# Kernel optimization log

Measured on AMD Instinct MI355X. Metric: run time of the kernel, lower is better.

The kernel has to match this reference:

```python
import jax, jax.numpy as jnp
import numpy as np

TEMP = 0.1
EPS = 1e-9  # torch CosineSimilarity eps


def setup_inputs() -> dict:
    key = jax.random.key(0)
    k1, k2 = jax.random.split(key)
    h = jax.random.normal(k1, (16384, 2048), dtype=jnp.float32)
    W = jax.random.normal(k2, (512, 2048), dtype=jnp.float32) * (1.0 / np.sqrt(2048))
    return {"h": h, "W": W}


def reference(h, W):
    # process_reps: h already 2D -> identity. Split into anchor / context halves.
    B = h.shape[0] // 2
    wz = h[:B] @ W.T      # [B, low_rank_dim]
    wc = h[B:] @ W.T      # [B, low_rank_dim]

    # CosineSimilarity(dim=-1, eps=1e-9): dot / max(||z||*||c||, eps), pairwise BxB
    nz = jnp.linalg.norm(wz, axis=-1)  # [B]
    nc = jnp.linalg.norm(wc, axis=-1)  # [B]
    sim = (wz @ wc.T) / jnp.maximum(nz[:, None] * nc[None, :], EPS)  # [B, B]
    sim = sim / TEMP

    sim_mean = sim.mean()
    sim_pos = jnp.diagonal(sim).mean()
    logprob = -jax.nn.log_softmax(sim, axis=1)
    loss = jnp.diagonal(logprob).mean()
    # matches loss_dict entries: {'loss', 'loss_pos', 'loss_neg'}
    return jnp.stack([loss, sim_pos, sim_mean])
```

## Files before the change

kernel.cpp:

```cpp
#include <hip/hip_runtime.h>


typedef __attribute__((ext_vector_type(8))) short bf16x8;
typedef __attribute__((ext_vector_type(4))) float floatx4;
typedef unsigned char uchar;

__device__ __forceinline__ unsigned short f2bf(float f) {
    union { float f; unsigned u; } v; v.f = f;
    unsigned r = (v.u + 0x7FFFu + ((v.u >> 16) & 1u)) >> 16;
    return (unsigned short)r;
}

__device__ __forceinline__ void async_copy16(const void* g, void* l) {
    __builtin_amdgcn_global_load_lds(
        (const __attribute__((address_space(1))) void*)g,
        (__attribute__((address_space(3))) void*)l,
        16, 0, 0);
}

__device__ __forceinline__ void cvt16(const float4* f, uchar* dst) {
    int4 pk;
    pk.x = (__builtin_amdgcn_cvt_pk_fp8_f32(f[0].x, f[0].y, 0, 0) & 0xffff)
         | (__builtin_amdgcn_cvt_pk_fp8_f32(f[0].z, f[0].w, 0, 0) << 16);
    pk.y = (__builtin_amdgcn_cvt_pk_fp8_f32(f[1].x, f[1].y, 0, 0) & 0xffff)
         | (__builtin_amdgcn_cvt_pk_fp8_f32(f[1].z, f[1].w, 0, 0) << 16);
    pk.z = (__builtin_amdgcn_cvt_pk_fp8_f32(f[2].x, f[2].y, 0, 0) & 0xffff)
         | (__builtin_amdgcn_cvt_pk_fp8_f32(f[2].z, f[2].w, 0, 0) << 16);
    pk.w = (__builtin_amdgcn_cvt_pk_fp8_f32(f[3].x, f[3].y, 0, 0) & 0xffff)
         | (__builtin_amdgcn_cvt_pk_fp8_f32(f[3].z, f[3].w, 0, 0) << 16);
    *reinterpret_cast<int4*>(dst) = pk;
}

__global__ __launch_bounds__(256) void cast_fp8_kernel(
    const float* __restrict__ src, uchar* __restrict__ dst, int n, float scale)
{
    const int i = (blockIdx.x * 256 + threadIdx.x) * 8;
    if (i + 7 < n) {
        float4 a = *reinterpret_cast<const float4*>(src + i);
        float4 b = *reinterpret_cast<const float4*>(src + i + 4);
        const int p01 = __builtin_amdgcn_cvt_pk_fp8_f32(a.x * scale, a.y * scale, 0, 0);
        const int p23 = __builtin_amdgcn_cvt_pk_fp8_f32(a.z * scale, a.w * scale, 0, 0);
        const int p45 = __builtin_amdgcn_cvt_pk_fp8_f32(b.x * scale, b.y * scale, 0, 0);
        const int p67 = __builtin_amdgcn_cvt_pk_fp8_f32(b.z * scale, b.w * scale, 0, 0);
        int2 w;
        w.x = (p01 & 0xffff) | (p23 << 16);
        w.y = (p45 & 0xffff) | (p67 << 16);
        *reinterpret_cast<int2*>(dst + i) = w;
    }
}

__device__ __forceinline__ size_t fl_off(int row_g, int col_g) {
    const int g = row_g >> 4, r15 = row_g & 15;
    const int c = col_g >> 5, q = (col_g >> 3) & 3, b = col_g & 7;
    return ((size_t)g * 16 + c) * 512 + (size_t)(q * 16 + r15) * 8 + b;
}

#define G1F_BODY(K, FC, FN, AR, BR, AW, BW, VM, STAGE_B, STAGE_H)              \
  {                                                                            \
    asm volatile("s_waitcnt vmcnt(" #VM ")" ::: "memory");                     \
    asm volatile("s_waitcnt lgkmcnt(0)" ::: "memory");                         \
    __builtin_amdgcn_s_barrier();                                              \
    __builtin_amdgcn_sched_barrier(0);                                         \
    long av[2][4], bv[2][8];                                                   \
    _Pragma("unroll")                                                          \
    for (int c = 0; c < 2; c++) {                                              \
      _Pragma("unroll")                                                        \
      for (int i = 0; i < 4; i++)                                              \
        av[c][i] = *reinterpret_cast<const long*>(AR + fA + i * 1024 + c * 32);\
      _Pragma("unroll")                                                        \
      for (int j = 0; j < 8; j++)                                              \
        bv[c][j] = *reinterpret_cast<const long*>(BR + fB + j * 1024 + c * 32);\
    }                                                                          \
    __builtin_amdgcn_s_setprio(1);                                             \
    _Pragma("unroll")                                                          \
    for (int c = 0; c < 2; c++)                                                \
      _Pragma("unroll")                                                        \
      for (int i = 0; i < 4; i++)                                              \
        _Pragma("unroll")                                                      \
        for (int j = 0; j < 8; j++)                                            \
          acc[i][j] = __builtin_amdgcn_mfma_f32_16x16x32_fp8_fp8(              \
              av[c][i], bv[c][j], acc[i][j], 0, 0, 0);                         \
    __builtin_amdgcn_s_setprio(0);                                             \
    if (STAGE_B) {                                                             \
      _Pragma("unroll")                                                        \
      for (int s = 0; s < 8; s++)                                              \
        async_copy16(gBs + ((K) + 1) * 64 + s * 131072, BW + swave + s * 4096);\
      cvt16(FC, AW + aoff);                                                    \
    }                                                                          \
    if (STAGE_H) {                                                             \
      _Pragma("unroll")                                                        \
      for (int c4 = 0; c4 < 4; c4++)                                           \
        FN[c4] = *reinterpret_cast<const float4*>(gH + ((K) + 2) * 64 + c4 * 4);\
    }                                                                          \
  }

__global__ __launch_bounds__(256, 1) void g1f(
    const float* __restrict__ h, const uchar* __restrict__ W8,
    uchar* __restrict__ Z8F, float* __restrict__ norm2)
{
    __shared__ __align__(16) uchar As0[64 * 64],  As1[64 * 64];
    __shared__ __align__(16) uchar Bs0[512 * 64], Bs1[512 * 64];

    const int blk = blockIdx.x;
    const int t = threadIdx.x;
    const int wave = t >> 6, lane = t & 63;
    const int quad = lane >> 4, l15 = lane & 15;

    floatx4 acc[4][8];
    #pragma unroll
    for (int i = 0; i < 4; i++)
        #pragma unroll
        for (int j = 0; j < 8; j++) acc[i][j] = {0.f, 0.f, 0.f, 0.f};

    const int arow = t >> 2, ap = t & 3;
    const float* gH = h + (size_t)(blk * 64 + arow) * 2048 + ap * 16;
    const int aoff = arow * 64 + ap * 16;

    const uchar* gBs = W8 + (size_t)(wave * 16 + (lane >> 2)) * 2048 + (lane & 3) * 16;
    const int swave = wave * 1024;

    const int fA = l15 * 64 + quad * 8;
    const int fB = wave * 8192 + l15 * 64 + quad * 8;

    #pragma unroll
    for (int s = 0; s < 8; s++)
        async_copy16(gBs + s * 131072, Bs0 + swave + s * 4096);
    float4 p0[4], f0[4], f1[4];
    #pragma unroll
    for (int c = 0; c < 4; c++) p0[c] = *reinterpret_cast<const float4*>(gH + c * 4);
    #pragma unroll
    for (int c = 0; c < 4; c++) f1[c] = *reinterpret_cast<const float4*>(gH + 64 + c * 4);
    cvt16(p0, As0 + aoff);

    for (int kb = 0; kb < 15; kb++) {
        const int k = kb * 2;
        G1F_BODY(k,     f1, f0, As0, Bs0, As1, Bs1, 4, 1, 1)
        G1F_BODY(k + 1, f0, f1, As1, Bs1, As0, Bs0, 4, 1, 1)
    }
    G1F_BODY(30, f1, f0, As0, Bs0, As1, Bs1, 4, 1, 0)
    G1F_BODY(31, f0, f1, As1, Bs1, As0, Bs0, 0, 0, 0)

    #pragma unroll
    for (int i = 0; i < 4; i++) {
        #pragma unroll
        for (int r = 0; r < 4; r++) {
            const int row_g = blk * 64 + i * 16 + quad * 4 + r;
            float pw = 0.f;
            #pragma unroll
            for (int jp = 0; jp < 4; jp++) {
                const int pk = __builtin_amdgcn_cvt_pk_fp8_f32(
                    acc[i][2 * jp][r], acc[i][2 * jp + 1][r], 0, 0);
                Z8F[fl_off(row_g, wave * 128 + (2 * jp) * 16 + l15)]     = (uchar)(pk & 0xff);
                Z8F[fl_off(row_g, wave * 128 + (2 * jp + 1) * 16 + l15)] = (uchar)((pk >> 8) & 0xff);
                const float q0 = __builtin_amdgcn_cvt_f32_fp8(pk, 0);
                const float q1 = __builtin_amdgcn_cvt_f32_fp8(pk, 1);
                pw += q0 * q0 + q1 * q1;
            }
            pw += __shfl_xor(pw, 1, 16);
            pw += __shfl_xor(pw, 2, 16);
            pw += __shfl_xor(pw, 4, 16);
            pw += __shfl_xor(pw, 8, 16);
            if (l15 == 0) atomicAdd(&norm2[row_g], pw);
        }
    }
}

__global__ __launch_bounds__(256) void g1_slow(
    const float* __restrict__ h, const float* __restrict__ W,
    uchar* __restrict__ Z8F, float* __restrict__ norm2)
{
    __shared__ __align__(16) unsigned short As[128][40];
    __shared__ __align__(16) unsigned short Bs[128][40];

    const int bn = blockIdx.x, bm = blockIdx.y;
    const int t = threadIdx.x;
    const int wave = t >> 6, lane = t & 63;
    const int wm = wave & 1, wn = wave >> 1;
    const int quad = lane >> 4, l15 = lane & 15;

    floatx4 acc[4][4];
    #pragma unroll
    for (int i = 0; i < 4; i++)
        #pragma unroll
        for (int j = 0; j < 4; j++) acc[i][j] = {0.f, 0.f, 0.f, 0.f};

    const int lrow = t >> 1, lhalf = t & 1;
    const float* ga = h + (size_t)(bm * 128 + lrow) * 2048 + lhalf * 16;
    const float* gb = W + (size_t)(bn * 128 + lrow) * 2048 + lhalf * 16;

    for (int k0 = 0; k0 < 2048; k0 += 32) {
        #pragma unroll
        for (int c = 0; c < 4; c++) {
            const float4 va = *reinterpret_cast<const float4*>(ga + k0 + c * 4);
            const float4 vb = *reinterpret_cast<const float4*>(gb + k0 + c * 4);
            ushort4 ua = make_ushort4(f2bf(va.x), f2bf(va.y), f2bf(va.z), f2bf(va.w));
            ushort4 ub = make_ushort4(f2bf(vb.x), f2bf(vb.y), f2bf(vb.z), f2bf(vb.w));
            *reinterpret_cast<ushort4*>(&As[lrow][lhalf * 16 + c * 4]) = ua;
            *reinterpret_cast<ushort4*>(&Bs[lrow][lhalf * 16 + c * 4]) = ub;
        }
        __syncthreads();
        bf16x8 af[4], bfr[4];
        #pragma unroll
        for (int i = 0; i < 4; i++)
            af[i] = *reinterpret_cast<const bf16x8*>(&As[wm * 64 + i * 16 + l15][quad * 8]);
        #pragma unroll
        for (int j = 0; j < 4; j++)
            bfr[j] = *reinterpret_cast<const bf16x8*>(&Bs[wn * 64 + j * 16 + l15][quad * 8]);
        #pragma unroll
        for (int i = 0; i < 4; i++)
            #pragma unroll
            for (int j = 0; j < 4; j++)
                acc[i][j] = __builtin_amdgcn_mfma_f32_16x16x32_bf16(af[i], bfr[j], acc[i][j], 0, 0, 0);
        __syncthreads();
    }

    #pragma unroll
    for (int i = 0; i < 4; i++) {
        #pragma unroll
        for (int r = 0; r < 4; r++) {
            const int row_g = bm * 128 + wm * 64 + i * 16 + quad * 4 + r;
            const int pk01 = __builtin_amdgcn_cvt_pk_fp8_f32(acc[i][0][r], acc[i][1][r], 0, 0);
            const int pk23 = __builtin_amdgcn_cvt_pk_fp8_f32(acc[i][2][r], acc[i][3][r], 0, 0);
            const uchar q8[4] = { (uchar)(pk01 & 0xff), (uchar)((pk01 >> 8) & 0xff),
                                  (uchar)(pk23 & 0xff), (uchar)((pk23 >> 8) & 0xff) };
            #pragma unroll
            for (int j = 0; j < 4; j++) {
                const int col_g = bn * 128 + wn * 64 + j * 16 + l15;
                Z8F[fl_off(row_g, col_g)] = q8[j];
            }
            const float q0 = __builtin_amdgcn_cvt_f32_fp8(pk01, 0);
            const float q1 = __builtin_amdgcn_cvt_f32_fp8(pk01, 1);
            const float q2 = __builtin_amdgcn_cvt_f32_fp8(pk23, 0);
            const float q3 = __builtin_amdgcn_cvt_f32_fp8(pk23, 1);
            float pw = q0 * q0 + q1 * q1 + q2 * q2 + q3 * q3;
            pw += __shfl_xor(pw, 1, 16);
            pw += __shfl_xor(pw, 2, 16);
            pw += __shfl_xor(pw, 4, 16);
            pw += __shfl_xor(pw, 8, 16);
            if (l15 == 0) atomicAdd(&norm2[row_g], pw);
        }
    }
}

__global__ __launch_bounds__(256, 4) void g2_main(
    const uchar* __restrict__ Z8F, const float* __restrict__ norm2,
    float* __restrict__ rowse, float* __restrict__ bsum, float* __restrict__ bdiag)
{
    __shared__ __align__(16) uchar Bs[32768];
    __shared__ float red[8];
    float (*lds_red)[20] = (float (*)[20])(void*)Bs;

    const int o = blockIdx.y * 64 + blockIdx.x;
    const int xcd = o & 7, idx = o >> 3;
    const int bg = idx >> 7, r = idx & 127;
    const int bm = xcd * 8 + (r >> 4);
    const int bn = bg * 16 + (r & 15);
    const int t = threadIdx.x;
    const int wave = t >> 6, lane = t & 63;
    const int quad = lane >> 4, l15 = lane & 15;

    const uchar* gB = Z8F + (size_t)(512 + bn * 8) * 8192 + t * 16;
    #pragma unroll
    for (int s = 0; s < 8; s++)
        async_copy16(gB + s * 8192, &Bs[s * 4096 + wave * 1024]);

    floatx4 acc[2][8];
    #pragma unroll
    for (int i = 0; i < 2; i++)
        #pragma unroll
        for (int j = 0; j < 8; j++) acc[i][j] = {0.f, 0.f, 0.f, 0.f};

    const uchar* baseA = Z8F + (size_t)(bm * 8 + wave * 2) * 8192 + lane * 8;

    long ab[3][2];
    #pragma unroll
    for (int d = 0; d < 2; d++)
        #pragma unroll
        for (int i = 0; i < 2; i++)
            ab[d][i] = *reinterpret_cast<const long*>(baseA + i * 8192 + d * 512);

    __syncthreads();

    #pragma unroll
    for (int c = 0; c < 16; c++) {
        const int cl = c & 7;
        if (c < 14) {
            #pragma unroll
            for (int i = 0; i < 2; i++)
                ab[(c + 2) % 3][i] = *reinterpret_cast<const long*>(
                    baseA + i * 8192 + (c + 2) * 512);
        }
        long bb[8];
        #pragma unroll
        for (int j = 0; j < 8; j++)
            bb[j] = *reinterpret_cast<const long*>(&Bs[j * 4096 + cl * 512 + lane * 8]);
        __builtin_amdgcn_s_setprio(1);
        #pragma unroll
        for (int i = 0; i < 2; i++)
            #pragma unroll
            for (int j = 0; j < 8; j++)
                acc[i][j] = __builtin_amdgcn_mfma_f32_16x16x32_fp8_fp8(
                    ab[c % 3][i], bb[j], acc[i][j], 0, 0, 0);
        __builtin_amdgcn_s_setprio(0);
        if (c == 7) {
            __syncthreads();
            #pragma unroll
            for (int s = 0; s < 8; s++)
                async_copy16(gB + s * 8192 + 4096, &Bs[s * 4096 + wave * 1024]);
            __syncthreads();
        }
    }

    __syncthreads();

    float rc8[8];
    #pragma unroll
    for (int j = 0; j < 8; j++)
        rc8[j] = rsqrtf(fmaxf(norm2[8192 + bn * 128 + j * 16 + l15], 1e-30f));

    const bool diagblk = (bm == bn);
    float s_tot2 = 0.f, s_diag2 = 0.f;
    #pragma unroll
    for (int i = 0; i < 2; i++) {
        #pragma unroll
        for (int rr = 0; rr < 4; rr++) {
            const int row_t = wave * 32 + i * 16 + quad * 4 + rr;
            const float rzl2 = rsqrtf(fmaxf(norm2[bm * 128 + row_t], 1e-30f)) * 14.4269504089f;
            float rx = 0.f;
            #pragma unroll
            for (int j = 0; j < 8; j++) {
                const float sim2 = acc[i][j][rr] * rzl2 * rc8[j];
                s_tot2 += sim2;
                rx += exp2f(sim2);
                if (diagblk && j == wave * 2 + i && l15 == quad * 4 + rr)
                    s_diag2 += sim2;
            }
            lds_red[row_t][l15] = rx;
        }
    }
    __syncthreads();

    {
        const int row = t >> 1, half = t & 1;
        float v = 0.f;
        #pragma unroll
        for (int cc = 0; cc < 8; cc++) v += lds_red[row][half * 8 + cc];
        v += __shfl_xor(v, 1, 64);
        if (half == 0) atomicAdd(&rowse[bm * 128 + row], v);
    }

    #pragma unroll
    for (int off = 32; off; off >>= 1) {
        s_tot2  += __shfl_xor(s_tot2, off, 64);
        s_diag2 += __shfl_xor(s_diag2, off, 64);
    }
    if (lane == 0) { red[wave] = s_tot2; red[4 + wave] = s_diag2; }
    __syncthreads();
    if (t == 0) {
        bsum[bm * 64 + bn]  = (red[0] + red[1] + red[2] + red[3]) * 0.69314718056f;
        bdiag[bm * 64 + bn] = (red[4] + red[5] + red[6] + red[7]) * 0.69314718056f;
    }
}

__global__ __launch_bounds__(256) void finalize_kernel(
    const float* __restrict__ rowse, const float* __restrict__ bsum,
    const float* __restrict__ bdiag, float* __restrict__ out)
{
    float a = 0.f, b = 0.f, c = 0.f;
    for (int i = threadIdx.x; i < 8192; i += 256) a += logf(rowse[i]);
    for (int i = threadIdx.x; i < 4096; i += 256) { b += bsum[i]; c += bdiag[i]; }
    #pragma unroll
    for (int off = 32; off; off >>= 1) {
        a += __shfl_xor(a, off, 64);
        b += __shfl_xor(b, off, 64);
        c += __shfl_xor(c, off, 64);
    }
    __shared__ float ra[4], rb[4], rc[4];
    const int wave = threadIdx.x >> 6, lane = threadIdx.x & 63;
    if (lane == 0) { ra[wave] = a; rb[wave] = b; rc[wave] = c; }
    __syncthreads();
    if (threadIdx.x == 0) {
        const float A = ra[0] + ra[1] + ra[2] + ra[3];
        const float B = rb[0] + rb[1] + rb[2] + rb[3];
        const float C = rc[0] + rc[1] + rc[2] + rc[3];
        const float diag_mean = C / 8192.f;
        out[0] = A / 8192.f - diag_mean;
        out[1] = diag_mean;
        out[2] = B / (8192.f * 8192.f);
    }
}

extern "C" void kernel_launch(void* const* d_in, const int* in_sizes, int n_in,
                              void* d_out, int out_size, void* d_ws, size_t ws_size,
                              hipStream_t stream) {
    const float* h = (const float*)d_in[0];
    const float* W = (const float*)d_in[1];
    float* out = (float*)d_out;

    char* ws = (char*)d_ws;
    float* norm2 = (float*)(ws);
    float* rowse = (float*)(ws + 65536);
    float* bsum  = (float*)(ws + 98304);
    float* bdiag = (float*)(ws + 114688);
    uchar* Z8F   = (uchar*)(ws + 131072);
    uchar* W8    = (uchar*)(ws + 8519680);
    const size_t NEED_FAST = 9568256ull;

    hipMemsetAsync(ws, 0, 131072, stream);

    if (ws_size >= NEED_FAST) {
        const int nw = 512 * 2048;
        hipLaunchKernelGGL(cast_fp8_kernel, dim3(nw / 2048), dim3(256), 0, stream, W, W8, nw, 32.0f);
        hipLaunchKernelGGL(g1f, dim3(256), dim3(256), 0, stream, h, W8, Z8F, norm2);
    } else {
        hipLaunchKernelGGL(g1_slow, dim3(4, 128), dim3(256), 0, stream, h, W, Z8F, norm2);
    }
    hipLaunchKernelGGL(g2_main, dim3(64, 64), dim3(256), 0, stream, Z8F, norm2, rowse, bsum, bdiag);
    hipLaunchKernelGGL(finalize_kernel, dim3(1), dim3(256), 0, stream, rowse, bsum, bdiag, out);
}
```

Baseline: 317.8 us.

## Pre-swizzle W into MFMA fragment layout and read B directly from global

```diff
diff --git a/kernel.cpp b/kernel.cpp
--- a/kernel.cpp
+++ b/kernel.cpp
@@ -18,35 +18,13 @@
         16, 0, 0);
 }
 
-__device__ __forceinline__ void cvt16(const float4* f, uchar* dst) {
-    int4 pk;
+__device__ __forceinline__ void cvt8(const float4* f, uchar* dst) {
+    int2 pk;
     pk.x = (__builtin_amdgcn_cvt_pk_fp8_f32(f[0].x, f[0].y, 0, 0) & 0xffff)
          | (__builtin_amdgcn_cvt_pk_fp8_f32(f[0].z, f[0].w, 0, 0) << 16);
     pk.y = (__builtin_amdgcn_cvt_pk_fp8_f32(f[1].x, f[1].y, 0, 0) & 0xffff)
          | (__builtin_amdgcn_cvt_pk_fp8_f32(f[1].z, f[1].w, 0, 0) << 16);
-    pk.z = (__builtin_amdgcn_cvt_pk_fp8_f32(f[2].x, f[2].y, 0, 0) & 0xffff)
-         | (__builtin_amdgcn_cvt_pk_fp8_f32(f[2].z, f[2].w, 0, 0) << 16);
-    pk.w = (__builtin_amdgcn_cvt_pk_fp8_f32(f[3].x, f[3].y, 0, 0) & 0xffff)
-         | (__builtin_amdgcn_cvt_pk_fp8_f32(f[3].z, f[3].w, 0, 0) << 16);
-    *reinterpret_cast<int4*>(dst) = pk;
-}
-
-__global__ __launch_bounds__(256) void cast_fp8_kernel(
-    const float* __restrict__ src, uchar* __restrict__ dst, int n, float scale)
-{
-    const int i = (blockIdx.x * 256 + threadIdx.x) * 8;
-    if (i + 7 < n) {
-        float4 a = *reinterpret_cast<const float4*>(src + i);
-        float4 b = *reinterpret_cast<const float4*>(src + i + 4);
-        const int p01 = __builtin_amdgcn_cvt_pk_fp8_f32(a.x * scale, a.y * scale, 0, 0);
-        const int p23 = __builtin_amdgcn_cvt_pk_fp8_f32(a.z * scale, a.w * scale, 0, 0);
-        const int p45 = __builtin_amdgcn_cvt_pk_fp8_f32(b.x * scale, b.y * scale, 0, 0);
-        const int p67 = __builtin_amdgcn_cvt_pk_fp8_f32(b.z * scale, b.w * scale, 0, 0);
-        int2 w;
-        w.x = (p01 & 0xffff) | (p23 << 16);
-        w.y = (p45 & 0xffff) | (p67 << 16);
-        *reinterpret_cast<int2*>(dst + i) = w;
-    }
+    *reinterpret_cast<int2*>(dst) = pk;
 }
 
 __device__ __forceinline__ size_t fl_off(int row_g, int col_g) {
@@ -55,21 +33,46 @@
     return ((size_t)g * 16 + c) * 512 + (size_t)(q * 16 + r15) * 8 + b;
 }
 
-#define G1F_BODY(K, FC, FN, AR, BR, AW, BW, VM, STAGE_B, STAGE_H)              \
+__global__ __launch_bounds__(256) void cast_w_frag(
+    const float* __restrict__ W, uchar* __restrict__ W8F)
+{
+    const int i = (blockIdx.x * 256 + threadIdx.x) * 8;
+    const int r = i >> 11, k = i & 2047;
+    const float* s = W + (size_t)r * 2048 + k;
+    float4 a = *reinterpret_cast<const float4*>(s);
+    float4 b = *reinterpret_cast<const float4*>(s + 4);
+    int2 w;
+    w.x = (__builtin_amdgcn_cvt_pk_fp8_f32(a.x * 32.f, a.y * 32.f, 0, 0) & 0xffff)
+        | (__builtin_amdgcn_cvt_pk_fp8_f32(a.z * 32.f, a.w * 32.f, 0, 0) << 16);
+    w.y = (__builtin_amdgcn_cvt_pk_fp8_f32(b.x * 32.f, b.y * 32.f, 0, 0) & 0xffff)
+        | (__builtin_amdgcn_cvt_pk_fp8_f32(b.z * 32.f, b.w * 32.f, 0, 0) << 16);
+    const size_t off = (size_t)(r >> 4) * 32768 + (size_t)(k >> 5) * 512
+                     + (size_t)((k >> 3) & 3) * 128 + (size_t)(r & 15) * 8;
+    *reinterpret_cast<int2*>(W8F + off) = w;
+}
+
+#define G1R_ITER(K, AsR, AsW, FC, FN, DO_CVT, DO_LOAD)                         \
   {                                                                            \
-    asm volatile("s_waitcnt vmcnt(" #VM ")" ::: "memory");                     \
-    asm volatile("s_waitcnt lgkmcnt(0)" ::: "memory");                         \
-    __builtin_amdgcn_s_barrier();                                              \
-    __builtin_amdgcn_sched_barrier(0);                                         \
-    long av[2][4], bv[2][8];                                                   \
+    __syncthreads();                                                           \
+    long av[4][2];                                                             \
     _Pragma("unroll")                                                          \
-    for (int c = 0; c < 2; c++) {                                              \
+    for (int i = 0; i < 4; i++)                                                \
       _Pragma("unroll")                                                        \
-      for (int i = 0; i < 4; i++)                                              \
-        av[c][i] = *reinterpret_cast<const long*>(AR + fA + i * 1024 + c * 32);\
+      for (int c = 0; c < 2; c++)                                              \
+        av[i][c] = *reinterpret_cast<const long*>(                             \
+            AsR + (i * 16 + l15) * 64 +                                        \
+            (((c * 2 + (quad >> 1)) ^ (l15 & 3)) << 4) + (quad & 1) * 8);      \
+    long bb[4][2];                                                             \
+    _Pragma("unroll")                                                          \
+    for (int j = 0; j < 4; j++)                                                \
       _Pragma("unroll")                                                        \
-      for (int j = 0; j < 8; j++)                                              \
-        bv[c][j] = *reinterpret_cast<const long*>(BR + fB + j * 1024 + c * 32);\
+      for (int c = 0; c < 2; c++)                                              \
+        bb[j][c] = *reinterpret_cast<const long*>(                             \
+            gWF + j * 32768 + ((K) * 2 + c) * 512);                            \
+    if (DO_CVT) cvt8(FC, AsW + adst);                                          \
+    if (DO_LOAD) {                                                             \
+      FN[0] = *reinterpret_cast<const float4*>(gH + ((K) + 2) * 64);           \
+      FN[1] = *reinterpret_cast<const float4*>(gH + ((K) + 2) * 64 + 4);       \
     }                                                                          \
     __builtin_amdgcn_s_setprio(1);                                             \
     _Pragma("unroll")                                                          \
@@ -77,68 +80,49 @@
       _Pragma("unroll")                                                        \
       for (int i = 0; i < 4; i++)                                              \
         _Pragma("unroll")                                                      \
-        for (int j = 0; j < 8; j++)                                            \
+        for (int j = 0; j < 4; j++)                                            \
           acc[i][j] = __builtin_amdgcn_mfma_f32_16x16x32_fp8_fp8(              \
-              av[c][i], bv[c][j], acc[i][j], 0, 0, 0);                         \
+              av[i][c], bb[j][c], acc[i][j], 0, 0, 0);                         \
     __builtin_amdgcn_s_setprio(0);                                             \
-    if (STAGE_B) {                                                             \
-      _Pragma("unroll")                                                        \
-      for (int s = 0; s < 8; s++)                                              \
-        async_copy16(gBs + ((K) + 1) * 64 + s * 131072, BW + swave + s * 4096);\
-      cvt16(FC, AW + aoff);                                                    \
-    }                                                                          \
-    if (STAGE_H) {                                                             \
-      _Pragma("unroll")                                                        \
-      for (int c4 = 0; c4 < 4; c4++)                                           \
-        FN[c4] = *reinterpret_cast<const float4*>(gH + ((K) + 2) * 64 + c4 * 4);\
-    }                                                                          \
   }
 
-__global__ __launch_bounds__(256, 1) void g1f(
-    const float* __restrict__ h, const uchar* __restrict__ W8,
+__global__ __launch_bounds__(512, 2) void g1r(
+    const float* __restrict__ h, const uchar* __restrict__ W8F,
     uchar* __restrict__ Z8F, float* __restrict__ norm2)
 {
-    __shared__ __align__(16) uchar As0[64 * 64],  As1[64 * 64];
-    __shared__ __align__(16) uchar Bs0[512 * 64], Bs1[512 * 64];
+    __shared__ __align__(16) uchar As0[64 * 64], As1[64 * 64];
 
     const int blk = blockIdx.x;
     const int t = threadIdx.x;
     const int wave = t >> 6, lane = t & 63;
     const int quad = lane >> 4, l15 = lane & 15;
 
-    floatx4 acc[4][8];
+    floatx4 acc[4][4];
     #pragma unroll
     for (int i = 0; i < 4; i++)
         #pragma unroll
-        for (int j = 0; j < 8; j++) acc[i][j] = {0.f, 0.f, 0.f, 0.f};
-
-    const int arow = t >> 2, ap = t & 3;
-    const float* gH = h + (size_t)(blk * 64 + arow) * 2048 + ap * 16;
-    const int aoff = arow * 64 + ap * 16;
-
-    const uchar* gBs = W8 + (size_t)(wave * 16 + (lane >> 2)) * 2048 + (lane & 3) * 16;
-    const int swave = wave * 1024;
-
-    const int fA = l15 * 64 + quad * 8;
-    const int fB = wave * 8192 + l15 * 64 + quad * 8;
-
-    #pragma unroll
-    for (int s = 0; s < 8; s++)
-        async_copy16(gBs + s * 131072, Bs0 + swave + s * 4096);
-    float4 p0[4], f0[4], f1[4];
-    #pragma unroll
-    for (int c = 0; c < 4; c++) p0[c] = *reinterpret_cast<const float4*>(gH + c * 4);
-    #pragma unroll
-    for (int c = 0; c < 4; c++) f1[c] = *reinterpret_cast<const float4*>(gH + 64 + c * 4);
-    cvt16(p0, As0 + aoff);
+        for (int j = 0; j < 4; j++) acc[i][j] = {0.f, 0.f, 0.f, 0.f};
+
+    const int arow = t >> 3, u = t & 7;
+    const float* gH = h + (size_t)(blk * 64 + arow) * 2048 + u * 8;
+    const int adst = arow * 64 + (((u >> 1) ^ (arow & 3)) << 4) + (u & 1) * 8;
+
+    const uchar* gWF = W8F + (size_t)(wave * 4) * 32768 + lane * 8;
+
+    float4 f0[2], f1[2];
+    f0[0] = *reinterpret_cast<const float4*>(gH);
+    f0[1] = *reinterpret_cast<const float4*>(gH + 4);
+    cvt8(f0, As0 + adst);
+    f1[0] = *reinterpret_cast<const float4*>(gH + 64);
+    f1[1] = *reinterpret_cast<const float4*>(gH + 68);
 
     for (int kb = 0; kb < 15; kb++) {
         const int k = kb * 2;
-        G1F_BODY(k,     f1, f0, As0, Bs0, As1, Bs1, 4, 1, 1)
-        G1F_BODY(k + 1, f0, f1, As1, Bs1, As0, Bs0, 4, 1, 1)
-    }
-    G1F_BODY(30, f1, f0, As0, Bs0, As1, Bs1, 4, 1, 0)
-    G1F_BODY(31, f0, f1, As1, Bs1, As0, Bs0, 0, 0, 0)
+        G1R_ITER(k,     As0, As1, f1, f0, 1, 1)
+        G1R_ITER(k + 1, As1, As0, f0, f1, 1, 1)
+    }
+    G1R_ITER(30, As0, As1, f1, f0, 1, 0)
+    G1R_ITER(31, As1, As0, f0, f1, 0, 0)
 
     #pragma unroll
     for (int i = 0; i < 4; i++) {
@@ -147,11 +131,11 @@
             const int row_g = blk * 64 + i * 16 + quad * 4 + r;
             float pw = 0.f;
             #pragma unroll
-            for (int jp = 0; jp < 4; jp++) {
+            for (int jp = 0; jp < 2; jp++) {
                 const int pk = __builtin_amdgcn_cvt_pk_fp8_f32(
                     acc[i][2 * jp][r], acc[i][2 * jp + 1][r], 0, 0);
-                Z8F[fl_off(row_g, wave * 128 + (2 * jp) * 16 + l15)]     = (uchar)(pk & 0xff);
-                Z8F[fl_off(row_g, wave * 128 + (2 * jp + 1) * 16 + l15)] = (uchar)((pk >> 8) & 0xff);
+                Z8F[fl_off(row_g, (wave * 4 + 2 * jp) * 16 + l15)]     = (uchar)(pk & 0xff);
+                Z8F[fl_off(row_g, (wave * 4 + 2 * jp + 1) * 16 + l15)] = (uchar)((pk >> 8) & 0xff);
                 const float q0 = __builtin_amdgcn_cvt_f32_fp8(pk, 0);
                 const float q1 = __builtin_amdgcn_cvt_f32_fp8(pk, 1);
                 pw += q0 * q0 + q1 * q1;
@@ -403,15 +387,14 @@
     float* bsum  = (float*)(ws + 98304);
     float* bdiag = (float*)(ws + 114688);
     uchar* Z8F   = (uchar*)(ws + 131072);
-    uchar* W8    = (uchar*)(ws + 8519680);
+    uchar* W8F   = (uchar*)(ws + 8519680);
     const size_t NEED_FAST = 9568256ull;
 
     hipMemsetAsync(ws, 0, 131072, stream);
 
     if (ws_size >= NEED_FAST) {
-        const int nw = 512 * 2048;
-        hipLaunchKernelGGL(cast_fp8_kernel, dim3(nw / 2048), dim3(256), 0, stream, W, W8, nw, 32.0f);
-        hipLaunchKernelGGL(g1f, dim3(256), dim3(256), 0, stream, h, W8, Z8F, norm2);
+        hipLaunchKernelGGL(cast_w_frag, dim3(512), dim3(256), 0, stream, W, W8F);
+        hipLaunchKernelGGL(g1r, dim3(256), dim3(512), 0, stream, h, W8F, Z8F, norm2);
     } else {
         hipLaunchKernelGGL(g1_slow, dim3(4, 128), dim3(256), 0, stream, h, W, Z8F, norm2);
     }
```

Result: faster. 284.7 us (-10.4%).
